# Kernel optimization log

Hardware: AMD Instinct MI355X
Metric: run time of the kernel (lower is better)

## Reference

```python
import jax, jax.numpy as jnp
import numpy as np

N = 50000
E = 800000
IN_FEAT = 128
HIDDEN = 64
HEADS = 4
CLASSES = 40
NEG_SLOPE = 0.2


def setup_inputs() -> dict:
    key = jax.random.key(0)
    ks = jax.random.split(key, 12)
    x = jax.random.normal(ks[0], (N, IN_FEAT), dtype=jnp.float32)
    # edge_index without self loops (module removes then re-adds them)
    src = jax.random.randint(ks[1], (E,), 0, N)
    off = jax.random.randint(ks[2], (E,), 1, N)
    dst = (src + off) % N  # guaranteed dst != src
    edge_index = jnp.stack([src, dst]).astype(jnp.int64)
    g = 1.0 / np.sqrt(IN_FEAT)
    lin1_w = jax.random.normal(ks[3], (IN_FEAT, HEADS * HIDDEN), dtype=jnp.float32) * g
    lin1_b = jax.random.normal(ks[4], (HEADS * HIDDEN,), dtype=jnp.float32) * 0.01
    att1 = jax.random.normal(ks[5], (1, HEADS, 2 * HIDDEN), dtype=jnp.float32) * (1.0 / np.sqrt(2 * HIDDEN))
    bias1 = jnp.zeros((HEADS * HIDDEN,), dtype=jnp.float32)
    lin2_w = jax.random.normal(ks[6], (HEADS * HIDDEN, CLASSES), dtype=jnp.float32) * (1.0 / np.sqrt(HEADS * HIDDEN))
    lin2_b = jax.random.normal(ks[7], (CLASSES,), dtype=jnp.float32) * 0.01
    att2 = jax.random.normal(ks[8], (1, 1, 2 * CLASSES), dtype=jnp.float32) * (1.0 / np.sqrt(2 * CLASSES))
    bias2 = jnp.zeros((CLASSES,), dtype=jnp.float32)
    return {"x": x, "edge_index": edge_index, "lin1_w": lin1_w, "lin1_b": lin1_b,
            "att1": att1, "bias1": bias1, "lin2_w": lin2_w, "lin2_b": lin2_b,
            "att2": att2, "bias2": bias2}


def gat_conv(x, src, dst, W, b_lin, att, bias, heads, oc):
    n = x.shape[0]
    fea = (x @ W + b_lin).reshape(n, heads, oc)            # [N, H, C]
    # attention logits: (cat([x_i, x_j]) * att).sum(-1) decomposed per node
    score_i = jnp.einsum('nhc,hc->nh', fea, att[0, :, :oc])  # target half
    score_j = jnp.einsum('nhc,hc->nh', fea, att[0, :, oc:])  # source half
    alpha = score_i[dst] + score_j[src]                    # [E, H]
    alpha = jax.nn.leaky_relu(alpha, NEG_SLOPE)
    # segment softmax over target node
    amax = jax.ops.segment_max(alpha, dst, num_segments=n)
    alpha = jnp.exp(alpha - amax[dst])
    asum = jax.ops.segment_sum(alpha, dst, num_segments=n)
    alpha = alpha / (asum[dst] + 1e-16)
    # message = x_j * alpha; scatter-add to target
    msg = fea[src] * alpha[:, :, None]                     # [E, H, C]
    out = jax.ops.segment_sum(msg, dst, num_segments=n)
    return out.reshape(n, heads * oc) + bias               # concat=True


def reference(x, edge_index, lin1_w, lin1_b, att1, bias1, lin2_w, lin2_b, att2, bias2):
    n = x.shape[0]
    loop = jnp.arange(n, dtype=edge_index.dtype)
    src = jnp.concatenate([edge_index[0], loop])  # add self loops
    dst = jnp.concatenate([edge_index[1], loop])
    h = gat_conv(x, src, dst, lin1_w, lin1_b, att1, bias1, HEADS, HIDDEN)
    h = jax.nn.relu(h)
    h = gat_conv(h, src, dst, lin2_w, lin2_b, att2, bias2, 1, CLASSES)
    return jax.nn.softmax(h, axis=1)
```

## Files before the change

### kernel.cpp

```cpp
#include <hip/hip_runtime.h>
#include <hip/hip_fp16.h>

#define NN 50000
#define NE 800000
#define INFEAT 128
#define F1 256
#define HID 64
#define CLS 40
#define NEGS 0.2f
#define NB 49

__device__ __forceinline__ float lrelu(float x) { return x > 0.0f ? x : NEGS * x; }

struct alignas(8) H4 { __half2 a, b; };
struct alignas(16) H8 { __half2 a, b, c, d; };

#define BM 128
#define BN2 128
#define BK 32
__global__ __launch_bounds__(256) void gemm1_k(const float* __restrict__ A,
                                               const float* __restrict__ W,
                                               const float* __restrict__ b,
                                               const float* __restrict__ att1,
                                               __half* __restrict__ feah,
                                               float* __restrict__ sI,
                                               float* __restrict__ sJ) {
    __shared__ float As[BK][BM + 4];
    __shared__ float Bs[BK][BN2 + 4];
    int tid = threadIdx.x;
    int row0 = blockIdx.x * BM;
    int colB = blockIdx.y * BN2;
    int tx = tid & 15, ty = tid >> 4;
    int ar = tid >> 3;
    int ac = (tid & 7) * 4;
    int bkr = tid >> 5;
    int bkc = (tid & 31) * 4;
    float4 pa[4], pb[4];
    auto load_tile = [&](int k0) {
        #pragma unroll
        for (int i = 0; i < 4; ++i) {
            int grow = row0 + ar + i * 32;
            pa[i] = (grow < NN) ? *(const float4*)&A[(size_t)grow * INFEAT + k0 + ac]
                                : make_float4(0.f, 0.f, 0.f, 0.f);
        }
        #pragma unroll
        for (int i = 0; i < 4; ++i)
            pb[i] = *(const float4*)&W[(size_t)(k0 + bkr + i * 8) * F1 + colB + bkc];
    };
    float acc[8][8] = {};
    load_tile(0);
    for (int k0 = 0; k0 < INFEAT; k0 += BK) {
        #pragma unroll
        for (int i = 0; i < 4; ++i) {
            int rr = ar + i * 32;
            As[ac + 0][rr] = pa[i].x; As[ac + 1][rr] = pa[i].y;
            As[ac + 2][rr] = pa[i].z; As[ac + 3][rr] = pa[i].w;
        }
        #pragma unroll
        for (int i = 0; i < 4; ++i)
            *(float4*)&Bs[bkr + i * 8][bkc] = pb[i];
        __syncthreads();
        if (k0 + BK < INFEAT) load_tile(k0 + BK);
        #pragma unroll
        for (int k = 0; k < BK; ++k) {
            float4 a0 = *(const float4*)&As[k][ty * 8];
            float4 a1 = *(const float4*)&As[k][ty * 8 + 4];
            float4 b0 = *(const float4*)&Bs[k][tx * 8];
            float4 b1 = *(const float4*)&Bs[k][tx * 8 + 4];
            float a[8] = {a0.x, a0.y, a0.z, a0.w, a1.x, a1.y, a1.z, a1.w};
            float bb[8] = {b0.x, b0.y, b0.z, b0.w, b1.x, b1.y, b1.z, b1.w};
            #pragma unroll
            for (int i = 0; i < 8; ++i)
                #pragma unroll
                for (int j = 0; j < 8; ++j) acc[i][j] += a[i] * bb[j];
        }
        __syncthreads();
    }
    int head = blockIdx.y * 2 + (tx >> 3);
    int colb = colB + tx * 8;
    int cin  = (tx & 7) * 8;
    float4 bv0 = *(const float4*)&b[colb];
    float4 bv1 = *(const float4*)&b[colb + 4];
    float bias8[8] = {bv0.x, bv0.y, bv0.z, bv0.w, bv1.x, bv1.y, bv1.z, bv1.w};
    float aI[8], aJ[8];
    #pragma unroll
    for (int j = 0; j < 8; ++j) {
        aI[j] = att1[head * 2 * HID + cin + j];
        aJ[j] = att1[head * 2 * HID + HID + cin + j];
    }
    #pragma unroll
    for (int i = 0; i < 8; ++i) {
        int grow = row0 + ty * 8 + i;
        float o[8];
        #pragma unroll
        for (int j = 0; j < 8; ++j) o[j] = acc[i][j] + bias8[j];
        if (grow < NN) {
            H8 v;
            v.a = __floats2half2_rn(o[0], o[1]);
            v.b = __floats2half2_rn(o[2], o[3]);
            v.c = __floats2half2_rn(o[4], o[5]);
            v.d = __floats2half2_rn(o[6], o[7]);
            *(H8*)&feah[(size_t)grow * F1 + colb] = v;
        }
        float sIp = 0.f, sJp = 0.f;
        #pragma unroll
        for (int j = 0; j < 8; ++j) { sIp += o[j] * aI[j]; sJp += o[j] * aJ[j]; }
        #pragma unroll
        for (int off = 1; off < 8; off <<= 1) {
            sIp += __shfl_xor(sIp, off);
            sJp += __shfl_xor(sJp, off);
        }
        if ((tx & 7) == 0 && grow < NN) {
            sI[grow * 4 + head] = sIp;
            sJ[grow * 4 + head] = sJp;
        }
    }
}

__global__ void hist_k(const int* __restrict__ dst, int* __restrict__ deg,
                       int* __restrict__ ord) {
    int e = blockIdx.x * blockDim.x + threadIdx.x;
    if (e < NE) ord[e] = atomicAdd(&deg[dst[e]], 1);
}

__global__ __launch_bounds__(1024) void scan1_k(const int* __restrict__ deg,
                                                int* __restrict__ row_off,
                                                int* __restrict__ bsum) {
    __shared__ int tmp[1024];
    int tid = threadIdx.x;
    int gid = blockIdx.x * 1024 + tid;
    int v = (gid < NN) ? deg[gid] : 0;
    tmp[tid] = v;
    __syncthreads();
    #pragma unroll
    for (int off = 1; off < 1024; off <<= 1) {
        int t = (tid >= off) ? tmp[tid - off] : 0;
        __syncthreads();
        tmp[tid] += t;
        __syncthreads();
    }
    if (gid < NN) row_off[gid] = tmp[tid] - v;
    if (tid == 1023) bsum[blockIdx.x] = tmp[1023];
}

__global__ void scan2_k(const int* __restrict__ bsum, int* __restrict__ bpref) {
    int tid = threadIdx.x;
    int orig = (tid < NB) ? bsum[tid] : 0;
    int v = orig;
    #pragma unroll
    for (int off = 1; off < 64; off <<= 1) {
        int t = __shfl_up(v, off);
        if (tid >= off) v += t;
    }
    if (tid < NB) bpref[tid] = v - orig;
}

__global__ __launch_bounds__(1024) void scan3_k(int* __restrict__ row_off,
                                                const int* __restrict__ bpref) {
    int gid = blockIdx.x * 1024 + threadIdx.x;
    if (gid < NN) row_off[gid] += bpref[blockIdx.x];
    if (gid == 0) row_off[NN] = NE;
}

__global__ void scatter_k(const int* __restrict__ src, const int* __restrict__ dst,
                          const int* __restrict__ ord, const int* __restrict__ row_off,
                          const float* __restrict__ sI, const float* __restrict__ sJ,
                          int* __restrict__ csr, float4* __restrict__ ep4) {
    int e = blockIdx.x * blockDim.x + threadIdx.x;
    if (e >= NE) return;
    int s = src[e], d = dst[e];
    int pos = row_off[d] + ord[e];
    float4 si = *(const float4*)&sI[d * 4];
    float4 sj = *(const float4*)&sJ[s * 4];
    float4 r;
    r.x = __expf(lrelu(si.x + sj.x));
    r.y = __expf(lrelu(si.y + sj.y));
    r.z = __expf(lrelu(si.z + sj.z));
    r.w = __expf(lrelu(si.w + sj.w));
    csr[pos] = s;
    ep4[pos] = r;
}

__global__ __launch_bounds__(256, 6) void agg1_k(const __half* __restrict__ feah,
                                                 const float* __restrict__ sI,
                                                 const float* __restrict__ sJ,
                                                 const float* __restrict__ epf,
                                                 const int* __restrict__ row_off,
                                                 const int* __restrict__ csr,
                                                 const float* __restrict__ bias,
                                                 float* __restrict__ out) {
    int wid = threadIdx.x >> 6, lane = threadIdx.x & 63;
    int n = blockIdx.x * 4 + wid;
    if (n >= NN) return;
    int h = lane >> 4;
    int c = lane * 4;
    float p = __expf(lrelu(sI[n * 4 + h] + sJ[n * 4 + h]));
    float asum = p;
    H4 vs = *(const H4*)&feah[(size_t)n * F1 + c];
    float2 sx = __half22float2(vs.a), sy = __half22float2(vs.b);
    float4 acc = make_float4(sx.x * p, sx.y * p, sy.x * p, sy.y * p);
    int beg = row_off[n], end = row_off[n + 1];
    int e = beg;
    for (; e + 8 <= end; e += 8) {
        int s0 = csr[e + 0], s1 = csr[e + 1], s2 = csr[e + 2], s3 = csr[e + 3];
        int s4 = csr[e + 4], s5 = csr[e + 5], s6 = csr[e + 6], s7 = csr[e + 7];
        float p0 = epf[(e + 0) * 4 + h], p1 = epf[(e + 1) * 4 + h];
        float p2 = epf[(e + 2) * 4 + h], p3 = epf[(e + 3) * 4 + h];
        float p4 = epf[(e + 4) * 4 + h], p5 = epf[(e + 5) * 4 + h];
        float p6 = epf[(e + 6) * 4 + h], p7 = epf[(e + 7) * 4 + h];
        H4 v0 = *(const H4*)&feah[(size_t)s0 * F1 + c];
        H4 v1 = *(const H4*)&feah[(size_t)s1 * F1 + c];
        H4 v2 = *(const H4*)&feah[(size_t)s2 * F1 + c];
        H4 v3 = *(const H4*)&feah[(size_t)s3 * F1 + c];
        H4 v4 = *(const H4*)&feah[(size_t)s4 * F1 + c];
        H4 v5 = *(const H4*)&feah[(size_t)s5 * F1 + c];
        H4 v6 = *(const H4*)&feah[(size_t)s6 * F1 + c];
        H4 v7 = *(const H4*)&feah[(size_t)s7 * F1 + c];
        asum += ((p0 + p1) + (p2 + p3)) + ((p4 + p5) + (p6 + p7));
        float2 x0 = __half22float2(v0.a), y0 = __half22float2(v0.b);
        float2 x1 = __half22float2(v1.a), y1 = __half22float2(v1.b);
        float2 x2 = __half22float2(v2.a), y2 = __half22float2(v2.b);
        float2 x3 = __half22float2(v3.a), y3 = __half22float2(v3.b);
        float2 x4 = __half22float2(v4.a), y4 = __half22float2(v4.b);
        float2 x5 = __half22float2(v5.a), y5 = __half22float2(v5.b);
        float2 x6 = __half22float2(v6.a), y6 = __half22float2(v6.b);
        float2 x7 = __half22float2(v7.a), y7 = __half22float2(v7.b);
        acc.x += (x0.x * p0 + x1.x * p1 + x2.x * p2 + x3.x * p3)
               + (x4.x * p4 + x5.x * p5 + x6.x * p6 + x7.x * p7);
        acc.y += (x0.y * p0 + x1.y * p1 + x2.y * p2 + x3.y * p3)
               + (x4.y * p4 + x5.y * p5 + x6.y * p6 + x7.y * p7);
        acc.z += (y0.x * p0 + y1.x * p1 + y2.x * p2 + y3.x * p3)
               + (y4.x * p4 + y5.x * p5 + y6.x * p6 + y7.x * p7);
        acc.w += (y0.y * p0 + y1.y * p1 + y2.y * p2 + y3.y * p3)
               + (y4.y * p4 + y5.y * p5 + y6.y * p6 + y7.y * p7);
    }
    for (; e + 4 <= end; e += 4) {
        int s0 = csr[e], s1 = csr[e + 1], s2 = csr[e + 2], s3 = csr[e + 3];
        float p0 = epf[(e + 0) * 4 + h], p1 = epf[(e + 1) * 4 + h];
        float p2 = epf[(e + 2) * 4 + h], p3 = epf[(e + 3) * 4 + h];
        H4 v0 = *(const H4*)&feah[(size_t)s0 * F1 + c];
        H4 v1 = *(const H4*)&feah[(size_t)s1 * F1 + c];
        H4 v2 = *(const H4*)&feah[(size_t)s2 * F1 + c];
        H4 v3 = *(const H4*)&feah[(size_t)s3 * F1 + c];
        asum += (p0 + p1) + (p2 + p3);
        float2 x0 = __half22float2(v0.a), y0 = __half22float2(v0.b);
        float2 x1 = __half22float2(v1.a), y1 = __half22float2(v1.b);
        float2 x2 = __half22float2(v2.a), y2 = __half22float2(v2.b);
        float2 x3 = __half22float2(v3.a), y3 = __half22float2(v3.b);
        acc.x += x0.x * p0 + x1.x * p1 + x2.x * p2 + x3.x * p3;
        acc.y += x0.y * p0 + x1.y * p1 + x2.y * p2 + x3.y * p3;
        acc.z += y0.x * p0 + y1.x * p1 + y2.x * p2 + y3.x * p3;
        acc.w += y0.y * p0 + y1.y * p1 + y2.y * p2 + y3.y * p3;
    }
    for (; e < end; ++e) {
        int s = csr[e];
        float pe = epf[e * 4 + h];
        asum += pe;
        H4 v = *(const H4*)&feah[(size_t)s * F1 + c];
        float2 x = __half22float2(v.a), y = __half22float2(v.b);
        acc.x += x.x * pe; acc.y += x.y * pe;
        acc.z += y.x * pe; acc.w += y.y * pe;
    }
    float inv = 1.0f / (asum + 1e-16f);
    float4 bv = *(const float4*)&bias[c];
    float4 o;
    o.x = fmaxf(acc.x * inv + bv.x, 0.f);
    o.y = fmaxf(acc.y * inv + bv.y, 0.f);
    o.z = fmaxf(acc.z * inv + bv.z, 0.f);
    o.w = fmaxf(acc.w * inv + bv.w, 0.f);
    *(float4*)&out[(size_t)n * F1 + c] = o;
}

#define G2N 102
__global__ __launch_bounds__(256) void gemm2_k(const float* __restrict__ h1,
                                               const float* __restrict__ W2,
                                               const float* __restrict__ b2,
                                               const float* __restrict__ att2,
                                               __half* __restrict__ fea2h,
                                               float* __restrict__ s2I,
                                               float* __restrict__ s2J) {
    __shared__ float Ws[F1 * CLS];
    __shared__ float redI[G2N][5];
    __shared__ float redJ[G2N][5];
    int tid = threadIdx.x;
    for (int i = tid * 4; i < F1 * CLS; i += 256 * 4)
        *(float4*)&Ws[i] = *(const float4*)&W2[i];
    __syncthreads();
    int nl = tid / 5, g = tid - nl * 5;
    int na = blockIdx.x * G2N + nl * 2;
    int nb = na + 1;
    bool actA = (tid < 255) && (na < NN);
    bool actB = (tid < 255) && (nb < NN);
    int c0 = g * 8;
    float accA[8] = {}, accB[8] = {};
    if (actA) {
        const float* rowA = h1 + (size_t)na * F1;
        const float* rowB = h1 + (size_t)(actB ? nb : na) * F1;
        for (int k = 0; k < F1; k += 4) {
            float4 ha = *(const float4*)&rowA[k];
            float4 hb = *(const float4*)&rowB[k];
            float a[4] = {ha.x, ha.y, ha.z, ha.w};
            float bl[4] = {hb.x, hb.y, hb.z, hb.w};
            #pragma unroll
            for (int kk = 0; kk < 4; ++kk) {
                float4 w0 = *(const float4*)&Ws[(k + kk) * CLS + c0];
                float4 w1 = *(const float4*)&Ws[(k + kk) * CLS + c0 + 4];
                accA[0] += a[kk] * w0.x; accA[1] += a[kk] * w0.y;
                accA[2] += a[kk] * w0.z; accA[3] += a[kk] * w0.w;
                accA[4] += a[kk] * w1.x; accA[5] += a[kk] * w1.y;
                accA[6] += a[kk] * w1.z; accA[7] += a[kk] * w1.w;
                accB[0] += bl[kk] * w0.x; accB[1] += bl[kk] * w0.y;
                accB[2] += bl[kk] * w0.z; accB[3] += bl[kk] * w0.w;
                accB[4] += bl[kk] * w1.x; accB[5] += bl[kk] * w1.y;
                accB[6] += bl[kk] * w1.z; accB[7] += bl[kk] * w1.w;
            }
        }
        float4 bb0 = *(const float4*)&b2[c0];
        float4 bb1 = *(const float4*)&b2[c0 + 4];
        float bias8[8] = {bb0.x, bb0.y, bb0.z, bb0.w, bb1.x, bb1.y, bb1.z, bb1.w};
        float sIa = 0.f, sJa = 0.f, sIb = 0.f, sJb = 0.f;
        #pragma unroll
        for (int j = 0; j < 8; ++j) {
            accA[j] += bias8[j];
            accB[j] += bias8[j];
            float aI = att2[c0 + j], aJ = att2[CLS + c0 + j];
            sIa += accA[j] * aI; sJa += accA[j] * aJ;
            sIb += accB[j] * aI; sJb += accB[j] * aJ;
        }
        H8 ha8;
        ha8.a = __floats2half2_rn(accA[0], accA[1]);
        ha8.b = __floats2half2_rn(accA[2], accA[3]);
        ha8.c = __floats2half2_rn(accA[4], accA[5]);
        ha8.d = __floats2half2_rn(accA[6], accA[7]);
        *(H8*)&fea2h[(size_t)na * CLS + c0] = ha8;
        redI[nl * 2][g] = sIa;
        redJ[nl * 2][g] = sJa;
        if (actB) {
            H8 hb8;
            hb8.a = __floats2half2_rn(accB[0], accB[1]);
            hb8.b = __floats2half2_rn(accB[2], accB[3]);
            hb8.c = __floats2half2_rn(accB[4], accB[5]);
            hb8.d = __floats2half2_rn(accB[6], accB[7]);
            *(H8*)&fea2h[(size_t)nb * CLS + c0] = hb8;
            redI[nl * 2 + 1][g] = sIb;
            redJ[nl * 2 + 1][g] = sJb;
        }
    }
    __syncthreads();
    if (actA && g == 0) {
        int r = nl * 2;
        s2I[na] = redI[r][0] + redI[r][1] + redI[r][2] + redI[r][3] + redI[r][4];
        s2J[na] = redJ[r][0] + redJ[r][1] + redJ[r][2] + redJ[r][3] + redJ[r][4];
        if (actB) {
            s2I[nb] = redI[r + 1][0] + redI[r + 1][1] + redI[r + 1][2] + redI[r + 1][3] + redI[r + 1][4];
            s2J[nb] = redJ[r + 1][0] + redJ[r + 1][1] + redJ[r + 1][2] + redJ[r + 1][3] + redJ[r + 1][4];
        }
    }
}

__global__ __launch_bounds__(256) void agg2_k(const __half* __restrict__ fea2h,
                                              const float* __restrict__ s2I,
                                              const float* __restrict__ s2J,
                                              const int* __restrict__ row_off,
                                              const int* __restrict__ csr,
                                              const float* __restrict__ bias2,
                                              float* __restrict__ out) {
    int wid = threadIdx.x >> 6, lane = threadIdx.x & 63;
    int n = blockIdx.x * 4 + wid;
    if (n >= NN) return;
    float si = s2I[n], sjn = s2J[n];
    int c = lane < CLS ? lane : 0;
    float p = __expf(lrelu(si + sjn));
    float asum = p;
    float acc = __half2float(fea2h[(size_t)n * CLS + c]) * p;
    int beg = row_off[n], end = row_off[n + 1];
    int e = beg;
    for (; e + 8 <= end; e += 8) {
        int s0 = csr[e + 0], s1 = csr[e + 1], s2 = csr[e + 2], s3 = csr[e + 3];
        int s4 = csr[e + 4], s5 = csr[e + 5], s6 = csr[e + 6], s7 = csr[e + 7];
        float a0 = s2J[s0], a1 = s2J[s1], a2 = s2J[s2], a3 = s2J[s3];
        float a4 = s2J[s4], a5 = s2J[s5], a6 = s2J[s6], a7 = s2J[s7];
        __half f0 = fea2h[(size_t)s0 * CLS + c];
        __half f1 = fea2h[(size_t)s1 * CLS + c];
        __half f2 = fea2h[(size_t)s2 * CLS + c];
        __half f3 = fea2h[(size_t)s3 * CLS + c];
        __half f4 = fea2h[(size_t)s4 * CLS + c];
        __half f5 = fea2h[(size_t)s5 * CLS + c];
        __half f6 = fea2h[(size_t)s6 * CLS + c];
        __half f7 = fea2h[(size_t)s7 * CLS + c];
        float p0 = __expf(lrelu(si + a0));
        float p1 = __expf(lrelu(si + a1));
        float p2 = __expf(lrelu(si + a2));
        float p3 = __expf(lrelu(si + a3));
        float p4 = __expf(lrelu(si + a4));
        float p5 = __expf(lrelu(si + a5));
        float p6 = __expf(lrelu(si + a6));
        float p7 = __expf(lrelu(si + a7));
        asum += ((p0 + p1) + (p2 + p3)) + ((p4 + p5) + (p6 + p7));
        acc += (__half2float(f0) * p0 + __half2float(f1) * p1
              + __half2float(f2) * p2 + __half2float(f3) * p3)
             + (__half2float(f4) * p4 + __half2float(f5) * p5
              + __half2float(f6) * p6 + __half2float(f7) * p7);
    }
    for (; e + 4 <= end; e += 4) {
        int s0 = csr[e], s1 = csr[e + 1], s2 = csr[e + 2], s3 = csr[e + 3];
        float p0 = __expf(lrelu(si + s2J[s0]));
        float p1 = __expf(lrelu(si + s2J[s1]));
        float p2 = __expf(lrelu(si + s2J[s2]));
        float p3 = __expf(lrelu(si + s2J[s3]));
        __half f0 = fea2h[(size_t)s0 * CLS + c];
        __half f1 = fea2h[(size_t)s1 * CLS + c];
        __half f2 = fea2h[(size_t)s2 * CLS + c];
        __half f3 = fea2h[(size_t)s3 * CLS + c];
        asum += (p0 + p1) + (p2 + p3);
        acc += __half2float(f0) * p0 + __half2float(f1) * p1
             + __half2float(f2) * p2 + __half2float(f3) * p3;
    }
    for (; e < end; ++e) {
        int s = csr[e];
        float pe = __expf(lrelu(si + s2J[s]));
        asum += pe;
        acc += __half2float(fea2h[(size_t)s * CLS + c]) * pe;
    }
    float row = acc / (asum + 1e-16f) + bias2[c];
    float v = (lane < CLS) ? row : -3.0e38f;
    float vm = v;
    #pragma unroll
    for (int off = 32; off; off >>= 1) vm = fmaxf(vm, __shfl_xor(vm, off));
    float ex = (lane < CLS) ? __expf(v - vm) : 0.f;
    float es = ex;
    #pragma unroll
    for (int off = 32; off; off >>= 1) es += __shfl_xor(es, off);
    if (lane < CLS) out[(size_t)n * CLS + lane] = ex / es;
}

extern "C" void kernel_launch(void* const* d_in, const int* in_sizes, int n_in,
                              void* d_out, int out_size, void* d_ws, size_t ws_size,
                              hipStream_t stream) {
    const float* x     = (const float*)d_in[0];
    const int*   ei    = (const int*)d_in[1];
    const float* w1    = (const float*)d_in[2];
    const float* b1    = (const float*)d_in[3];
    const float* att1  = (const float*)d_in[4];
    const float* bias1 = (const float*)d_in[5];
    const float* w2    = (const float*)d_in[6];
    const float* b2    = (const float*)d_in[7];
    const float* att2  = (const float*)d_in[8];
    const float* bias2 = (const float*)d_in[9];
    const int* src = ei;
    const int* dst = ei + NE;
    float* out = (float*)d_out;

    char* p = (char*)d_ws;
    auto alloc = [&](size_t bytes) {
        char* r = p;
        p += (bytes + 255) & ~(size_t)255;
        return r;
    };
    __half* fea1h = (__half*)alloc((size_t)NN * F1 * 2);
    float* h1     = (float*)alloc((size_t)NN * F1 * 4);
    float* sI1    = (float*)alloc((size_t)NN * 4 * 4);
    float* sJ1    = (float*)alloc((size_t)NN * 4 * 4);
    __half* fea2h = (__half*)alloc((size_t)NN * CLS * 2);
    float* s2I    = (float*)alloc((size_t)NN * 4);
    float* s2J    = (float*)alloc((size_t)NN * 4);
    int*   deg    = (int*)alloc((size_t)NN * 4);
    int*   row_off= (int*)alloc((size_t)(NN + 1) * 4);
    int*   bsum   = (int*)alloc((size_t)NB * 4);
    int*   bpref  = (int*)alloc((size_t)NB * 4);
    int*   ord    = (int*)alloc((size_t)NE * 4);
    int*   csr    = (int*)alloc((size_t)NE * 4);
    float* ep1    = (float*)alloc((size_t)NE * 4 * 4);

    hipMemsetAsync(deg, 0, (size_t)NN * 4, stream);

    dim3 g1((NN + BM - 1) / BM, F1 / BN2);
    gemm1_k<<<g1, 256, 0, stream>>>(x, w1, b1, att1, fea1h, sI1, sJ1);
    hist_k<<<(NE + 255) / 256, 256, 0, stream>>>(dst, deg, ord);
    scan1_k<<<NB, 1024, 0, stream>>>(deg, row_off, bsum);
    scan2_k<<<1, 64, 0, stream>>>(bsum, bpref);
    scan3_k<<<NB, 1024, 0, stream>>>(row_off, bpref);
    scatter_k<<<(NE + 255) / 256, 256, 0, stream>>>(src, dst, ord, row_off,
                                                    sI1, sJ1, csr, (float4*)ep1);
    agg1_k<<<(NN + 3) / 4, 256, 0, stream>>>(fea1h, sI1, sJ1, ep1, row_off, csr, bias1, h1);
    gemm2_k<<<(NN + G2N - 1) / G2N, 256, 0, stream>>>(h1, w2, b2, att2, fea2h, s2I, s2J);
    agg2_k<<<(NN + 3) / 4, 256, 0, stream>>>(fea2h, s2I, s2J, row_off, csr, bias2, out);
}
```

Measured before the change: 259.1 us.

## Rewrite layer-1 GEMM with fp16 MFMA instructions, one head per block

Replaces the fp32 register-tiled FMA GEMM for the first linear layer with an MFMA 16x16x32 f16 kernel. Inputs and weights are converted to half in shared memory, each block handles 128 rows of one head, and the attention-score reductions are redone with 16-lane shuffles. The goal is to move GEMM throughput onto the matrix cores. In exchange it drops the register prefetch double-buffering, reads W with strided scalar loads, stores feah as scalar half writes, and lowers input precision to fp16.

```diff
diff --git a/kernel.cpp b/kernel.cpp
--- a/kernel.cpp
+++ b/kernel.cpp
@@ -15,9 +15,10 @@
 struct alignas(8) H4 { __half2 a, b; };
 struct alignas(16) H8 { __half2 a, b, c, d; };
 
-#define BM 128
-#define BN2 128
-#define BK 32
+typedef __attribute__((ext_vector_type(8))) _Float16 f16x8;
+typedef __attribute__((ext_vector_type(4))) float f32x4;
+
+#define GBM 128
 __global__ __launch_bounds__(256) void gemm1_k(const float* __restrict__ A,
                                                const float* __restrict__ W,
                                                const float* __restrict__ b,
@@ -25,94 +26,95 @@
                                                __half* __restrict__ feah,
                                                float* __restrict__ sI,
                                                float* __restrict__ sJ) {
-    __shared__ float As[BK][BM + 4];
-    __shared__ float Bs[BK][BN2 + 4];
+    __shared__ __align__(16) _Float16 As[128][40];
+    __shared__ __align__(16) _Float16 Ws[64][40];
     int tid = threadIdx.x;
-    int row0 = blockIdx.x * BM;
-    int colB = blockIdx.y * BN2;
-    int tx = tid & 15, ty = tid >> 4;
-    int ar = tid >> 3;
-    int ac = (tid & 7) * 4;
-    int bkr = tid >> 5;
-    int bkc = (tid & 31) * 4;
-    float4 pa[4], pb[4];
-    auto load_tile = [&](int k0) {
+    int wid = tid >> 6, lane = tid & 63;
+    int row0 = blockIdx.x * GBM;
+    int head = blockIdx.y;
+    int colB = head * 64;
+    int lr = lane & 15;
+    int lg = lane >> 4;
+
+    f32x4 acc[2][4];
+    #pragma unroll
+    for (int rt = 0; rt < 2; ++rt)
+        #pragma unroll
+        for (int ct = 0; ct < 4; ++ct) acc[rt][ct] = (f32x4){0.f, 0.f, 0.f, 0.f};
+
+    int wcol = tid & 63;
+    int wkg  = tid >> 6;
+
+    for (int k0 = 0; k0 < INFEAT; k0 += 32) {
         #pragma unroll
         for (int i = 0; i < 4; ++i) {
-            int grow = row0 + ar + i * 32;
-            pa[i] = (grow < NN) ? *(const float4*)&A[(size_t)grow * INFEAT + k0 + ac]
-                                : make_float4(0.f, 0.f, 0.f, 0.f);
-        }
-        #pragma unroll
-        for (int i = 0; i < 4; ++i)
-            pb[i] = *(const float4*)&W[(size_t)(k0 + bkr + i * 8) * F1 + colB + bkc];
-    };
-    float acc[8][8] = {};
-    load_tile(0);
-    for (int k0 = 0; k0 < INFEAT; k0 += BK) {
+            int q = tid + 256 * i;
+            int r = q >> 3;
+            int c4 = (q & 7) * 4;
+            int grow = row0 + r;
+            float4 v = make_float4(0.f, 0.f, 0.f, 0.f);
+            if (grow < NN) v = *(const float4*)&A[(size_t)grow * INFEAT + k0 + c4];
+            As[r][c4 + 0] = (_Float16)v.x; As[r][c4 + 1] = (_Float16)v.y;
+            As[r][c4 + 2] = (_Float16)v.z; As[r][c4 + 3] = (_Float16)v.w;
+        }
+        {
+            f16x8 wv;
+            #pragma unroll
+            for (int j = 0; j < 8; ++j)
+                wv[j] = (_Float16)W[(size_t)(k0 + wkg * 8 + j) * F1 + colB + wcol];
+            *(f16x8*)&Ws[wcol][wkg * 8] = wv;
+        }
+        __syncthreads();
+        f16x8 afrag[2], bfrag[4];
+        #pragma unroll
+        for (int rt = 0; rt < 2; ++rt)
+            afrag[rt] = *(const f16x8*)&As[wid * 32 + rt * 16 + lr][lg * 8];
+        #pragma unroll
+        for (int ct = 0; ct < 4; ++ct)
+            bfrag[ct] = *(const f16x8*)&Ws[ct * 16 + lr][lg * 8];
+        #pragma unroll
+        for (int rt = 0; rt < 2; ++rt)
+            #pragma unroll
+            for (int ct = 0; ct < 4; ++ct)
+                acc[rt][ct] = __builtin_amdgcn_mfma_f32_16x16x32_f16(
+                    afrag[rt], bfrag[ct], acc[rt][ct], 0, 0, 0);
+        __syncthreads();
+    }
+    float aIv[4], aJv[4], bv[4];
+    #pragma unroll
+    for (int ct = 0; ct < 4; ++ct) {
+        int cin = ct * 16 + lr;
+        aIv[ct] = att1[head * 2 * HID + cin];
+        aJv[ct] = att1[head * 2 * HID + HID + cin];
+        bv[ct]  = b[colB + cin];
+    }
+    #pragma unroll
+    for (int rt = 0; rt < 2; ++rt) {
         #pragma unroll
         for (int i = 0; i < 4; ++i) {
-            int rr = ar + i * 32;
-            As[ac + 0][rr] = pa[i].x; As[ac + 1][rr] = pa[i].y;
-            As[ac + 2][rr] = pa[i].z; As[ac + 3][rr] = pa[i].w;
-        }
-        #pragma unroll
-        for (int i = 0; i < 4; ++i)
-            *(float4*)&Bs[bkr + i * 8][bkc] = pb[i];
-        __syncthreads();
-        if (k0 + BK < INFEAT) load_tile(k0 + BK);
-        #pragma unroll
-        for (int k = 0; k < BK; ++k) {
-            float4 a0 = *(const float4*)&As[k][ty * 8];
-            float4 a1 = *(const float4*)&As[k][ty * 8 + 4];
-            float4 b0 = *(const float4*)&Bs[k][tx * 8];
-            float4 b1 = *(const float4*)&Bs[k][tx * 8 + 4];
-            float a[8] = {a0.x, a0.y, a0.z, a0.w, a1.x, a1.y, a1.z, a1.w};
-            float bb[8] = {b0.x, b0.y, b0.z, b0.w, b1.x, b1.y, b1.z, b1.w};
+            int grow = row0 + wid * 32 + rt * 16 + lg * 4 + i;
+            float o[4];
+            float sIp = 0.f, sJp = 0.f;
             #pragma unroll
-            for (int i = 0; i < 8; ++i)
+            for (int ct = 0; ct < 4; ++ct) {
+                o[ct] = acc[rt][ct][i] + bv[ct];
+                sIp += o[ct] * aIv[ct];
+                sJp += o[ct] * aJv[ct];
+            }
+            #pragma unroll
+            for (int off = 1; off < 16; off <<= 1) {
+                sIp += __shfl_xor(sIp, off);
+                sJp += __shfl_xor(sJp, off);
+            }
+            if (grow < NN) {
                 #pragma unroll
-                for (int j = 0; j < 8; ++j) acc[i][j] += a[i] * bb[j];
-        }
-        __syncthreads();
-    }
-    int head = blockIdx.y * 2 + (tx >> 3);
-    int colb = colB + tx * 8;
-    int cin  = (tx & 7) * 8;
-    float4 bv0 = *(const float4*)&b[colb];
-    float4 bv1 = *(const float4*)&b[colb + 4];
-    float bias8[8] = {bv0.x, bv0.y, bv0.z, bv0.w, bv1.x, bv1.y, bv1.z, bv1.w};
-    float aI[8], aJ[8];
-    #pragma unroll
-    for (int j = 0; j < 8; ++j) {
-        aI[j] = att1[head * 2 * HID + cin + j];
-        aJ[j] = att1[head * 2 * HID + HID + cin + j];
-    }
-    #pragma unroll
-    for (int i = 0; i < 8; ++i) {
-        int grow = row0 + ty * 8 + i;
-        float o[8];
-        #pragma unroll
-        for (int j = 0; j < 8; ++j) o[j] = acc[i][j] + bias8[j];
-        if (grow < NN) {
-            H8 v;
-            v.a = __floats2half2_rn(o[0], o[1]);
-            v.b = __floats2half2_rn(o[2], o[3]);
-            v.c = __floats2half2_rn(o[4], o[5]);
-            v.d = __floats2half2_rn(o[6], o[7]);
-            *(H8*)&feah[(size_t)grow * F1 + colb] = v;
-        }
-        float sIp = 0.f, sJp = 0.f;
-        #pragma unroll
-        for (int j = 0; j < 8; ++j) { sIp += o[j] * aI[j]; sJp += o[j] * aJ[j]; }
-        #pragma unroll
-        for (int off = 1; off < 8; off <<= 1) {
-            sIp += __shfl_xor(sIp, off);
-            sJp += __shfl_xor(sJp, off);
-        }
-        if ((tx & 7) == 0 && grow < NN) {
-            sI[grow * 4 + head] = sIp;
-            sJ[grow * 4 + head] = sJp;
+                for (int ct = 0; ct < 4; ++ct)
+                    feah[(size_t)grow * F1 + colB + ct * 16 + lr] = __float2half(o[ct]);
+                if (lr == 0) {
+                    sI[grow * 4 + head] = sIp;
+                    sJ[grow * 4 + head] = sJp;
+                }
+            }
         }
     }
 }
@@ -474,7 +476,7 @@
 
     hipMemsetAsync(deg, 0, (size_t)NN * 4, stream);
 
-    dim3 g1((NN + BM - 1) / BM, F1 / BN2);
+    dim3 g1((NN + GBM - 1) / GBM, 4);
     gemm1_k<<<g1, 256, 0, stream>>>(x, w1, b1, att1, fea1h, sI1, sJ1);
     hist_k<<<(NE + 255) / 256, 256, 0, stream>>>(dst, deg, ord);
     scan1_k<<<NB, 1024, 0, stream>>>(deg, row_off, bsum);
```

Result: faster. 228.4 us (-11.9%).
